# Optimization experiments

Hardware: AMD Instinct MI355X
Metric: run time of the kernel (lower is better)

Reference implementation:

```python
import jax, jax.numpy as jnp
import numpy as np

N_NODES = 100000
N_EDGES = 1600000
F_IN, F_HID, F_OUT = 64, 64, 32


def setup_inputs() -> dict:
    key = jax.random.key(0)
    k1, k2, k3, k4 = jax.random.split(key, 4)
    x = jax.random.normal(k1, (N_NODES, F_IN), dtype=jnp.float32)
    edge_idx = jax.random.randint(k2, (2, N_EDGES), 0, N_NODES, dtype=jnp.int64)
    W1 = jax.random.normal(k3, (F_IN, F_HID), dtype=jnp.float32) * (1.0 / np.sqrt(F_IN))
    b1 = jnp.zeros((F_HID,), dtype=jnp.float32)
    W2 = jax.random.normal(k4, (F_HID, F_OUT), dtype=jnp.float32) * (1.0 / np.sqrt(F_HID))
    b2 = jnp.zeros((F_OUT,), dtype=jnp.float32)
    return {"x": x, "edge_idx": edge_idx, "W1": W1, "b1": b1, "W2": W2, "b2": b2}


def _gcn_conv(h, src, dst, norm, W, b, n):
    # PyG GCNConv: transform first, then normalized sum aggregation, then bias.
    h = h @ W                                   # [N, F_out]
    msg = h[src] * norm[:, None]                # [E+N, F_out] gather + scale
    agg = jax.ops.segment_sum(msg, dst, num_segments=n)  # scatter-add
    return agg + b


def reference(x, edge_idx, W1, b1, W2, b2):
    n = x.shape[0]
    loop = jnp.arange(n, dtype=edge_idx.dtype)
    src = jnp.concatenate([edge_idx[0], loop])  # add self-loops
    dst = jnp.concatenate([edge_idx[1], loop])
    # symmetric normalization D^-1/2 (A+I) D^-1/2
    deg = jax.ops.segment_sum(jnp.ones_like(dst, dtype=x.dtype), dst, num_segments=n)
    dinv = jnp.where(deg > 0, jax.lax.rsqrt(deg), 0.0)
    norm = dinv[src] * dinv[dst]                # [E+N]

    h = _gcn_conv(x, src, dst, norm, W1, b1, n)
    h = jax.nn.relu(h)
    # dropout(p=0.5) is identity in eval mode (deterministic reference)
    out = _gcn_conv(h, src, dst, norm, W2, b2, n)
    return out
```

## Files before the change

kernel.cpp:

```cpp
#include <hip/hip_runtime.h>
#include <hip/hip_bf16.h>
#include <hip/hip_fp16.h>


#define N_FEAT_IN 64
#define B2SHIFT 9
#define CHUNK 4096

struct alignas(8) half4 { __half2 lo, hi; };

__global__ __launch_bounds__(1024) void passA_hist(const int* __restrict__ dst,
                                                   int* __restrict__ H, int E) {
    __shared__ int h[256];
    int t = threadIdx.x;
    if (t < 256) h[t] = 0;
    __syncthreads();
    int base = blockIdx.x * CHUNK;
    int end = min(base + CHUNK, E);
    for (int i = base + t; i < end; i += 1024)
        atomicAdd(&h[dst[i] >> B2SHIFT], 1);
    __syncthreads();
    if (t < 256) H[blockIdx.x * 256 + t] = h[t];
}

__global__ __launch_bounds__(512) void col_scan_a(int* __restrict__ H,
                                                  int* __restrict__ ctot, int NR) {
    __shared__ int s[512];
    int b = blockIdx.x;
    int t = threadIdx.x;
    int v = (t < NR) ? H[t * 256 + b] : 0;
    s[t] = v;
    __syncthreads();
    for (int off = 1; off < 512; off <<= 1) {
        int a = (t >= off) ? s[t - off] : 0;
        __syncthreads();
        s[t] += a;
        __syncthreads();
    }
    if (t < NR) H[t * 256 + b] = s[t] - v;
    if (t == 511) ctot[b] = s[511];
}

__global__ __launch_bounds__(256) void col_scan_b(const int* __restrict__ ctot,
                                                  int* __restrict__ cbase,
                                                  int* __restrict__ bbase,
                                                  int* __restrict__ row_ptr,
                                                  int NB, int n, int E) {
    __shared__ int s[256];
    int t = threadIdx.x;
    int v = ctot[t];
    s[t] = v;
    __syncthreads();
    for (int off = 1; off < 256; off <<= 1) {
        int a = (t >= off) ? s[t - off] : 0;
        __syncthreads();
        s[t] += a;
        __syncthreads();
    }
    int e = s[t] - v;
    cbase[t] = e;
    if (t < NB) bbase[t] = e;
    if (t == 0) { bbase[NB] = E; row_ptr[n] = E; }
}

__global__ __launch_bounds__(1024) void passB_place(const int* __restrict__ src,
                                                    const int* __restrict__ dst,
                                                    const int* __restrict__ H,
                                                    const int* __restrict__ cbase,
                                                    unsigned* __restrict__ bedges, int E) {
    __shared__ int cur[256];
    int t = threadIdx.x;
    if (t < 256) cur[t] = H[blockIdx.x * 256 + t] + cbase[t];
    __syncthreads();
    int base = blockIdx.x * CHUNK;
    int end = min(base + CHUNK, E);
    for (int i = base + t; i < end; i += 1024) {
        int d = dst[i];
        int p = atomicAdd(&cur[d >> B2SHIFT], 1);
        bedges[p] = ((unsigned)src[i] << B2SHIFT) | (unsigned)(d & 511);
    }
}

__global__ __launch_bounds__(1024) void bucket_csr(const int* __restrict__ bbase,
                                                   const unsigned* __restrict__ bedges,
                                                   int* __restrict__ row_ptr,
                                                   float* __restrict__ dinv,
                                                   int* __restrict__ csr_src, int n) {
    __shared__ int lh[512];
    __shared__ int cur[512];
    int t = threadIdx.x;
    if (t < 512) lh[t] = 0;
    __syncthreads();
    int b = blockIdx.x;
    int beg = bbase[b], end = bbase[b + 1];
    for (int i = beg + t; i < end; i += 1024)
        atomicAdd(&lh[bedges[i] & 511], 1);
    __syncthreads();
    int c = (t < 512) ? lh[t] : 0;
    for (int off = 1; off < 512; off <<= 1) {
        int a = (t < 512 && t >= off) ? lh[t - off] : 0;
        __syncthreads();
        if (t < 512) lh[t] += a;
        __syncthreads();
    }
    if (t < 512) {
        int d = (b << B2SHIFT) + t;
        int excl = beg + lh[t] - c;
        cur[t] = excl;
        if (d < n) {
            row_ptr[d] = excl;
            dinv[d] = rsqrtf((float)c + 1.0f);
        }
    }
    __syncthreads();
    for (int i = beg + t; i < end; i += 1024) {
        unsigned v = bedges[i];
        int p = atomicAdd(&cur[v & 511], 1);
        csr_src[p] = (int)(v >> B2SHIFT);
    }
}

__global__ __launch_bounds__(256) void gemm64(const float* __restrict__ A,
                                              const float* __restrict__ W,
                                              const float* __restrict__ dinv,
                                              __half* __restrict__ outh, int n) {
    constexpr int K = 64, FO = 64, CPT = 16;
    __shared__ float As[64][K + 4];
    __shared__ float Ws[K][FO];

    const int t = threadIdx.x;
    const int r0 = blockIdx.x * 64;

    if (blockIdx.x == 0 && t < FO)
        outh[(size_t)n * FO + t] = __float2half(0.f);

    for (int i = t; i < K * FO / 4; i += 256) {
        int k = i / (FO / 4);
        int c4 = (i % (FO / 4)) * 4;
        *(float4*)&Ws[k][c4] = *(const float4*)&W[k * FO + c4];
    }
    for (int i = t; i < 1024; i += 256) {
        int row = i / 16;
        int c4 = (i % 16) * 4;
        int g = r0 + row;
        float4 v = make_float4(0.f, 0.f, 0.f, 0.f);
        if (g < n) v = *(const float4*)&A[(size_t)g * K + c4];
        *(float4*)&As[row][c4] = v;
    }
    __syncthreads();

    const int row = t >> 2;
    const int c0 = (t & 3) * CPT;
    float acc[CPT];
#pragma unroll
    for (int j = 0; j < CPT; ++j) acc[j] = 0.f;
#pragma unroll
    for (int k = 0; k < K; ++k) {
        float xv = As[row][k];
#pragma unroll
        for (int j = 0; j < CPT; ++j) acc[j] = fmaf(xv, Ws[k][c0 + j], acc[j]);
    }

    int g = r0 + row;
    if (g < n) {
        float sc = dinv[g];
#pragma unroll
        for (int j4 = 0; j4 < CPT; j4 += 4) {
            half4 h;
            h.lo = __floats2half2_rn(acc[j4] * sc, acc[j4 + 1] * sc);
            h.hi = __floats2half2_rn(acc[j4 + 2] * sc, acc[j4 + 3] * sc);
            *(half4*)&outh[(size_t)g * FO + c0 + j4] = h;
        }
    }
}

__global__ __launch_bounds__(256) void agg64(const int* __restrict__ row_ptr,
                                             const int* __restrict__ csr_src,
                                             const float* __restrict__ dinv,
                                             const __half* __restrict__ xs1,
                                             const float* __restrict__ b1,
                                             __half* __restrict__ th, int n) {
    int d = blockIdx.x * 16 + (threadIdx.x >> 4);
    if (d >= n) return;
    int c = threadIdx.x & 15;

    int beg = row_ptr[d];
    int end = row_ptr[d + 1];

    half4 sv = *(const half4*)&xs1[(size_t)d * 64 + 4 * c];
    float2 slo = __half22float2(sv.lo), shi = __half22float2(sv.hi);
    float a0 = slo.x, a1 = slo.y, a2 = shi.x, a3 = shi.y;

    for (int jb = beg; jb < end; jb += 8) {
        int idx[8];
#pragma unroll
        for (int k = 0; k < 8; ++k) {
            int j = jb + k;
            int s = csr_src[min(j, end - 1)];
            idx[k] = (j < end) ? s : n;
        }
        half4 v[8];
#pragma unroll
        for (int k = 0; k < 8; ++k)
            v[k] = *(const half4*)&xs1[(size_t)idx[k] * 64 + 4 * c];
#pragma unroll
        for (int k = 0; k < 8; ++k) {
            float2 lo = __half22float2(v[k].lo), hi = __half22float2(v[k].hi);
            a0 += lo.x; a1 += lo.y; a2 += hi.x; a3 += hi.y;
        }
    }

    float di = dinv[d];
    float4 bv = *(const float4*)&b1[4 * c];
    float t0 = fmaxf(fmaf(di, a0, bv.x), 0.f);
    float t1 = fmaxf(fmaf(di, a1, bv.y), 0.f);
    float t2 = fmaxf(fmaf(di, a2, bv.z), 0.f);
    float t3 = fmaxf(fmaf(di, a3, bv.w), 0.f);
    half4 h;
    h.lo = __floats2half2_rn(t0, t1);
    h.hi = __floats2half2_rn(t2, t3);
    *(half4*)&th[(size_t)d * 64 + 4 * c] = h;
}

__global__ __launch_bounds__(256) void gemm32h(const __half* __restrict__ Ah,
                                               const float* __restrict__ W,
                                               const float* __restrict__ dinv,
                                               __half* __restrict__ outh, int n) {
    constexpr int K = 64, FO = 32, CPT = 8;
    __shared__ float As[64][K + 4];
    __shared__ float Ws[K][FO];

    const int t = threadIdx.x;
    const int r0 = blockIdx.x * 64;

    if (blockIdx.x == 0 && t < FO)
        outh[(size_t)n * FO + t] = __float2half(0.f);

    for (int i = t; i < K * FO / 4; i += 256) {
        int k = i / (FO / 4);
        int c4 = (i % (FO / 4)) * 4;
        *(float4*)&Ws[k][c4] = *(const float4*)&W[k * FO + c4];
    }
    for (int i = t; i < 1024; i += 256) {
        int row = i / 16;
        int c4 = (i % 16) * 4;
        int g = r0 + row;
        float4 v = make_float4(0.f, 0.f, 0.f, 0.f);
        if (g < n) {
            half4 hv = *(const half4*)&Ah[(size_t)g * K + c4];
            float2 lo = __half22float2(hv.lo), hi = __half22float2(hv.hi);
            v = make_float4(lo.x, lo.y, hi.x, hi.y);
        }
        *(float4*)&As[row][c4] = v;
    }
    __syncthreads();

    const int row = t >> 2;
    const int c0 = (t & 3) * CPT;
    float acc[CPT];
#pragma unroll
    for (int j = 0; j < CPT; ++j) acc[j] = 0.f;
#pragma unroll
    for (int k = 0; k < K; ++k) {
        float xv = As[row][k];
#pragma unroll
        for (int j = 0; j < CPT; ++j) acc[j] = fmaf(xv, Ws[k][c0 + j], acc[j]);
    }

    int g = r0 + row;
    if (g < n) {
        float sc = dinv[g];
#pragma unroll
        for (int j4 = 0; j4 < CPT; j4 += 4) {
            half4 h;
            h.lo = __floats2half2_rn(acc[j4] * sc, acc[j4 + 1] * sc);
            h.hi = __floats2half2_rn(acc[j4 + 2] * sc, acc[j4 + 3] * sc);
            *(half4*)&outh[(size_t)g * FO + c0 + j4] = h;
        }
    }
}

__global__ __launch_bounds__(256) void agg32(const int* __restrict__ row_ptr,
                                             const int* __restrict__ csr_src,
                                             const float* __restrict__ dinv,
                                             const __half* __restrict__ xs2,
                                             const float* __restrict__ b2,
                                             float* __restrict__ out, int n) {
    int d = blockIdx.x * 32 + (threadIdx.x >> 3);
    if (d >= n) return;
    int c = threadIdx.x & 7;

    int beg = row_ptr[d];
    int end = row_ptr[d + 1];

    half4 sv = *(const half4*)&xs2[(size_t)d * 32 + 4 * c];
    float2 slo = __half22float2(sv.lo), shi = __half22float2(sv.hi);
    float a0 = slo.x, a1 = slo.y, a2 = shi.x, a3 = shi.y;

    for (int jb = beg; jb < end; jb += 8) {
        int idx[8];
#pragma unroll
        for (int k = 0; k < 8; ++k) {
            int j = jb + k;
            int s = csr_src[min(j, end - 1)];
            idx[k] = (j < end) ? s : n;
        }
        half4 v[8];
#pragma unroll
        for (int k = 0; k < 8; ++k)
            v[k] = *(const half4*)&xs2[(size_t)idx[k] * 32 + 4 * c];
#pragma unroll
        for (int k = 0; k < 8; ++k) {
            float2 lo = __half22float2(v[k].lo), hi = __half22float2(v[k].hi);
            a0 += lo.x; a1 += lo.y; a2 += hi.x; a3 += hi.y;
        }
    }

    float di = dinv[d];
    float4 bv = *(const float4*)&b2[4 * c];
    float4 r;
    r.x = fmaf(di, a0, bv.x);
    r.y = fmaf(di, a1, bv.y);
    r.z = fmaf(di, a2, bv.z);
    r.w = fmaf(di, a3, bv.w);
    *(float4*)&out[(size_t)d * 32 + 4 * c] = r;
}

extern "C" void kernel_launch(void* const* d_in, const int* in_sizes, int n_in,
                              void* d_out, int out_size, void* d_ws, size_t ws_size,
                              hipStream_t stream) {
    const float* x  = (const float*)d_in[0];
    const int*   ei = (const int*)d_in[1];
    const float* W1 = (const float*)d_in[2];
    const float* b1 = (const float*)d_in[3];
    const float* W2 = (const float*)d_in[4];
    const float* b2 = (const float*)d_in[5];
    float* out = (float*)d_out;

    const int n = in_sizes[0] / N_FEAT_IN;
    const int E = in_sizes[1] / 2;
    const int* srcI = ei;
    const int* dstI = ei + E;

    const int NB = (n + 511) >> B2SHIFT;
    const int NR = (E + CHUNK - 1) / CHUNK;

    char* ws = (char*)d_ws;
    size_t off = 0;
    auto alloc = [&](size_t bytes) {
        void* p = ws + off;
        off += (bytes + 255) & ~(size_t)255;
        return p;
    };
    float*    dinv    = (float*)alloc((size_t)n * 4);
    int*      row_ptr = (int*)alloc((size_t)(n + 1) * 4);
    int*      bbase   = (int*)alloc((size_t)(NB + 1) * 4);
    int*      ctot    = (int*)alloc((size_t)256 * 4);
    int*      cbase   = (int*)alloc((size_t)256 * 4);
    int*      H       = (int*)alloc((size_t)NR * 256 * 4);
    unsigned* bedges  = (unsigned*)alloc((size_t)E * 4);
    int*      csr_src = (int*)alloc((size_t)E * 4);
    __half*   xs1     = (__half*)alloc((size_t)(n + 1) * 64 * 2);
    __half*   th      = (__half*)alloc((size_t)n * 64 * 2);
    __half*   xs2     = (__half*)alloc((size_t)(n + 1) * 32 * 2);

    passA_hist<<<NR, 1024, 0, stream>>>(dstI, H, E);
    col_scan_a<<<256, 512, 0, stream>>>(H, ctot, NR);
    col_scan_b<<<1, 256, 0, stream>>>(ctot, cbase, bbase, row_ptr, NB, n, E);
    passB_place<<<NR, 1024, 0, stream>>>(srcI, dstI, H, cbase, bedges, E);

    bucket_csr<<<NB, 1024, 0, stream>>>(bbase, bedges, row_ptr, dinv, csr_src, n);

    gemm64<<<(n + 63) / 64, 256, 0, stream>>>(x, W1, dinv, xs1, n);

    agg64<<<(n + 15) / 16, 256, 0, stream>>>(row_ptr, csr_src, dinv, xs1, b1, th, n);

    gemm32h<<<(n + 63) / 64, 256, 0, stream>>>(th, W2, dinv, xs2, n);

    agg32<<<(n + 31) / 32, 256, 0, stream>>>(row_ptr, csr_src, dinv, xs2, b2, out, n);
}
```

Measured before the change: 203.4 us.

## Pad CSR rows to multiples of eight and widen aggregation gathers to 16 bytes

Each destination's neighbor list is padded to a multiple of 8 entries, with the padding pointing at a zero row, and a separate row-end array is kept. The aggregation kernels can then read indices as aligned int4 vectors without bounds checks and prefetch the next index block while gathering. Each thread now handles 8 features using 16-byte half8 loads instead of 4 with 8-byte loads, so fewer threads cover each node. The cost is a larger CSR buffer, extra padding writes in bucket_csr, and more wasted gathers on the padded zero rows.

```diff
diff --git a/kernel.cpp b/kernel.cpp
--- a/kernel.cpp
+++ b/kernel.cpp
@@ -6,8 +6,10 @@
 #define N_FEAT_IN 64
 #define B2SHIFT 9
 #define CHUNK 4096
+#define PADSTRIDE 3592
 
 struct alignas(8) half4 { __half2 lo, hi; };
+struct alignas(16) half8 { __half2 h[4]; };
 
 __global__ __launch_bounds__(1024) void passA_hist(const int* __restrict__ dst,
                                                    int* __restrict__ H, int E) {
@@ -84,6 +86,7 @@
 __global__ __launch_bounds__(1024) void bucket_csr(const int* __restrict__ bbase,
                                                    const unsigned* __restrict__ bedges,
                                                    int* __restrict__ row_ptr,
+                                                   int* __restrict__ rend,
                                                    float* __restrict__ dinv,
                                                    int* __restrict__ csr_src, int n) {
     __shared__ int lh[512];
@@ -97,19 +100,26 @@
         atomicAdd(&lh[bedges[i] & 511], 1);
     __syncthreads();
     int c = (t < 512) ? lh[t] : 0;
+    __syncthreads();
+    int cp = (c + 7) & ~7;
+    if (t < 512) lh[t] = cp;
+    __syncthreads();
     for (int off = 1; off < 512; off <<= 1) {
         int a = (t < 512 && t >= off) ? lh[t - off] : 0;
         __syncthreads();
         if (t < 512) lh[t] += a;
         __syncthreads();
     }
+    int pb = ((beg + 7) & ~7) + b * PADSTRIDE;
     if (t < 512) {
         int d = (b << B2SHIFT) + t;
-        int excl = beg + lh[t] - c;
-        cur[t] = excl;
+        int rbeg = pb + lh[t] - cp;
+        cur[t] = rbeg;
         if (d < n) {
-            row_ptr[d] = excl;
+            row_ptr[d] = rbeg;
+            rend[d] = rbeg + cp;
             dinv[d] = rsqrtf((float)c + 1.0f);
+            for (int i = c; i < cp; ++i) csr_src[rbeg + i] = n;
         }
     }
     __syncthreads();
@@ -174,52 +184,81 @@
     }
 }
 
+#define ACC8(v)                                                       \
+    {                                                                 \
+        float2 f0 = __half22float2((v).h[0]);                         \
+        float2 f1 = __half22float2((v).h[1]);                         \
+        float2 f2 = __half22float2((v).h[2]);                         \
+        float2 f3 = __half22float2((v).h[3]);                         \
+        a0 += f0.x; a1 += f0.y; a2 += f1.x; a3 += f1.y;               \
+        a4 += f2.x; a5 += f2.y; a6 += f3.x; a7 += f3.y;               \
+    }
+
 __global__ __launch_bounds__(256) void agg64(const int* __restrict__ row_ptr,
+                                             const int* __restrict__ rend,
                                              const int* __restrict__ csr_src,
                                              const float* __restrict__ dinv,
                                              const __half* __restrict__ xs1,
                                              const float* __restrict__ b1,
                                              __half* __restrict__ th, int n) {
-    int d = blockIdx.x * 16 + (threadIdx.x >> 4);
+    int d = blockIdx.x * 32 + (threadIdx.x >> 3);
     if (d >= n) return;
-    int c = threadIdx.x & 15;
+    int c = threadIdx.x & 7;
+    const half8* __restrict__ xrow = (const half8*)xs1 + c;
+
+    half8 sv = xrow[(size_t)d * 8];
+    float a0, a1, a2, a3, a4, a5, a6, a7;
+    {
+        float2 f0 = __half22float2(sv.h[0]), f1 = __half22float2(sv.h[1]);
+        float2 f2 = __half22float2(sv.h[2]), f3 = __half22float2(sv.h[3]);
+        a0 = f0.x; a1 = f0.y; a2 = f1.x; a3 = f1.y;
+        a4 = f2.x; a5 = f2.y; a6 = f3.x; a7 = f3.y;
+    }
 
     int beg = row_ptr[d];
-    int end = row_ptr[d + 1];
-
-    half4 sv = *(const half4*)&xs1[(size_t)d * 64 + 4 * c];
-    float2 slo = __half22float2(sv.lo), shi = __half22float2(sv.hi);
-    float a0 = slo.x, a1 = slo.y, a2 = shi.x, a3 = shi.y;
-
-    for (int jb = beg; jb < end; jb += 8) {
-        int idx[8];
-#pragma unroll
-        for (int k = 0; k < 8; ++k) {
-            int j = jb + k;
-            int s = csr_src[min(j, end - 1)];
-            idx[k] = (j < end) ? s : n;
-        }
-        half4 v[8];
-#pragma unroll
-        for (int k = 0; k < 8; ++k)
-            v[k] = *(const half4*)&xs1[(size_t)idx[k] * 64 + 4 * c];
-#pragma unroll
-        for (int k = 0; k < 8; ++k) {
-            float2 lo = __half22float2(v[k].lo), hi = __half22float2(v[k].hi);
-            a0 += lo.x; a1 += lo.y; a2 += hi.x; a3 += hi.y;
+    int end = rend[d];
+    if (beg < end) {
+        int4 ia = *(const int4*)&csr_src[beg];
+        int4 ib = *(const int4*)&csr_src[beg + 4];
+        int jb = beg;
+        for (;;) {
+            int jn = jb + 8;
+            bool more = jn < end;
+            int js = more ? jn : beg;
+            int4 na = *(const int4*)&csr_src[js];
+            int4 nb = *(const int4*)&csr_src[js + 4];
+            half8 v0 = xrow[(size_t)ia.x * 8];
+            half8 v1 = xrow[(size_t)ia.y * 8];
+            half8 v2 = xrow[(size_t)ia.z * 8];
+            half8 v3 = xrow[(size_t)ia.w * 8];
+            half8 v4 = xrow[(size_t)ib.x * 8];
+            half8 v5 = xrow[(size_t)ib.y * 8];
+            half8 v6 = xrow[(size_t)ib.z * 8];
+            half8 v7 = xrow[(size_t)ib.w * 8];
+            ACC8(v0); ACC8(v1); ACC8(v2); ACC8(v3);
+            ACC8(v4); ACC8(v5); ACC8(v6); ACC8(v7);
+            if (!more) break;
+            jb = jn; ia = na; ib = nb;
         }
     }
 
     float di = dinv[d];
-    float4 bv = *(const float4*)&b1[4 * c];
-    float t0 = fmaxf(fmaf(di, a0, bv.x), 0.f);
-    float t1 = fmaxf(fmaf(di, a1, bv.y), 0.f);
-    float t2 = fmaxf(fmaf(di, a2, bv.z), 0.f);
-    float t3 = fmaxf(fmaf(di, a3, bv.w), 0.f);
-    half4 h;
-    h.lo = __floats2half2_rn(t0, t1);
-    h.hi = __floats2half2_rn(t2, t3);
-    *(half4*)&th[(size_t)d * 64 + 4 * c] = h;
+    float4 ba = *(const float4*)&b1[8 * c];
+    float4 bb = *(const float4*)&b1[8 * c + 4];
+    float t0 = fmaxf(fmaf(di, a0, ba.x), 0.f);
+    float t1 = fmaxf(fmaf(di, a1, ba.y), 0.f);
+    float t2 = fmaxf(fmaf(di, a2, ba.z), 0.f);
+    float t3 = fmaxf(fmaf(di, a3, ba.w), 0.f);
+    float t4 = fmaxf(fmaf(di, a4, bb.x), 0.f);
+    float t5 = fmaxf(fmaf(di, a5, bb.y), 0.f);
+    float t6 = fmaxf(fmaf(di, a6, bb.z), 0.f);
+    float t7 = fmaxf(fmaf(di, a7, bb.w), 0.f);
+    half8 o;
+    o.h[0] = __floats2half2_rn(t0, t1);
+    o.h[1] = __floats2half2_rn(t2, t3);
+    o.h[2] = __floats2half2_rn(t4, t5);
+    o.h[3] = __floats2half2_rn(t6, t7);
+    *(half8*)&th[(size_t)d * 64 + 8 * c] = o;
 }
 
 __global__ __launch_bounds__(256) void gemm32h(const __half* __restrict__ Ah,
@@ -281,49 +320,67 @@
 }
 
 __global__ __launch_bounds__(256) void agg32(const int* __restrict__ row_ptr,
+                                             const int* __restrict__ rend,
                                              const int* __restrict__ csr_src,
                                              const float* __restrict__ dinv,
                                              const __half* __restrict__ xs2,
                                              const float* __restrict__ b2,
                                              float* __restrict__ out, int n) {
-    int d = blockIdx.x * 32 + (threadIdx.x >> 3);
+    int d = blockIdx.x * 64 + (threadIdx.x >> 2);
     if (d >= n) return;
-    int c = threadIdx.x & 7;
+    int c = threadIdx.x & 3;
+    const half8* __restrict__ xrow = (const half8*)xs2 + c;
+
+    half8 sv = xrow[(size_t)d * 4];
+    float a0, a1, a2, a3, a4, a5, a6, a7;
+    {
+        float2 f0 = __half22float2(sv.h[0]), f1 = __half22float2(sv.h[1]);
+        float2 f2 = __half22float2(sv.h[2]), f3 = __half22float2(sv.h[3]);
+        a0 = f0.x; a1 = f0.y; a2 = f1.x; a3 = f1.y;
+        a4 = f2.x; a5 = f2.y; a6 = f3.x; a7 = f3.y;
+    }
 
     int beg = row_ptr[d];
-    int end = row_ptr[d + 1];
-
-    half4 sv = *(const half4*)&xs2[(size_t)d * 32 + 4 * c];
-    float2 slo = __half22float2(sv.lo), shi = __half22float2(sv.hi);
-    float a0 = slo.x, a1 = slo.y, a2 = shi.x, a3 = shi.y;
-
-    for (int jb = beg; jb < end; jb += 8) {
-        int idx[8];
-#pragma unroll
-        for (int k = 0; k < 8; ++k) {
-            int j = jb + k;
-            int s = csr_src[min(j, end - 1)];
-            idx[k] = (j < end) ? s : n;
-        }
-        half4 v[8];
-#pragma unroll
-        for (int k = 0; k < 8; ++k)
-            v[k] = *(const half4*)&xs2[(size_t)idx[k] * 32 + 4 * c];
-#pragma unroll
-        for (int k = 0; k < 8; ++k) {
-            float2 lo = __half22float2(v[k].lo), hi = __half22float2(v[k].hi);
-            a0 += lo.x; a1 += lo.y; a2 += hi.x; a3 += hi.y;
+    int end = rend[d];
+    if (beg < end) {
+        int4 ia = *(const int4*)&csr_src[beg];
+        int4 ib = *(const int4*)&csr_src[beg + 4];
+        int jb = beg;
+        for (;;) {
+            int jn = jb + 8;
+            bool more = jn < end;
+            int js = more ? jn : beg;
+            int4 na = *(const int4*)&csr_src[js];
+            int4 nb = *(const int4*)&csr_src[js + 4];
+            half8 v0 = xrow[(size_t)ia.x * 4];
+            half8 v1 = xrow[(size_t)ia.y * 4];
+            half8 v2 = xrow[(size_t)ia.z * 4];
+            half8 v3 = xrow[(size_t)ia.w * 4];
+            half8 v4 = xrow[(size_t)ib.x * 4];
+            half8 v5 = xrow[(size_t)ib.y * 4];
+            half8 v6 = xrow[(size_t)ib.z * 4];
+            half8 v7 = xrow[(size_t)ib.w * 4];
+            ACC8(v0); ACC8(v1); ACC8(v2); ACC8(v3);
+            ACC8(v4); ACC8(v5); ACC8(v6); ACC8(v7);
+            if (!more) break;
+            jb = jn; ia = na; ib = nb;
         }
     }
 
     float di = dinv[d];
-    float4 bv = *(const float4*)&b2[4 * c];
-    float4 r;
-    r.x = fmaf(di, a0, bv.x);
-    r.y = fmaf(di, a1, bv.y);
-    r.z = fmaf(di, a2, bv.z);
-    r.w = fmaf(di, a3, bv.w);
-    *(float4*)&out[(size_t)d * 32 + 4 * c] = r;
+    float4 ba = *(const float4*)&b2[8 * c];
+    float4 bb = *(const float4*)&b2[8 * c + 4];
+    float4 r0, r1;
+    r0.x = fmaf(di, a0, ba.x);
+    r0.y = fmaf(di, a1, ba.y);
+    r0.z = fmaf(di, a2, ba.z);
+    r0.w = fmaf(di, a3, ba.w);
+    r1.x = fmaf(di, a4, bb.x);
+    r1.y = fmaf(di, a5, bb.y);
+    r1.z = fmaf(di, a6, bb.z);
+    r1.w = fmaf(di, a7, bb.w);
+    *(float4*)&out[(size_t)d * 32 + 8 * c] = r0;
+    *(float4*)&out[(size_t)d * 32 + 8 * c + 4] = r1;
 }
 
 extern "C" void kernel_launch(void* const* d_in, const int* in_sizes, int n_in,
@@ -354,12 +411,13 @@
     };
     float*    dinv    = (float*)alloc((size_t)n * 4);
     int*      row_ptr = (int*)alloc((size_t)(n + 1) * 4);
+    int*      rend    = (int*)alloc((size_t)n * 4);
     int*      bbase   = (int*)alloc((size_t)(NB + 1) * 4);
     int*      ctot    = (int*)alloc((size_t)256 * 4);
     int*      cbase   = (int*)alloc((size_t)256 * 4);
     int*      H       = (int*)alloc((size_t)NR * 256 * 4);
     unsigned* bedges  = (unsigned*)alloc((size_t)E * 4);
-    int*      csr_src = (int*)alloc((size_t)E * 4);
+    int*      csr_src = (int*)alloc((size_t)(E + (size_t)NB * PADSTRIDE + 16) * 4);
     __half*   xs1     = (__half*)alloc((size_t)(n + 1) * 64 * 2);
     __half*   th      = (__half*)alloc((size_t)n * 64 * 2);
     __half*   xs2     = (__half*)alloc((size_t)(n + 1) * 32 * 2);
@@ -369,13 +427,13 @@
     col_scan_b<<<1, 256, 0, stream>>>(ctot, cbase, bbase, row_ptr, NB, n, E);
     passB_place<<<NR, 1024, 0, stream>>>(srcI, dstI, H, cbase, bedges, E);
 
-    bucket_csr<<<NB, 1024, 0, stream>>>(bbase, bedges, row_ptr, dinv, csr_src, n);
+    bucket_csr<<<NB, 1024, 0, stream>>>(bbase, bedges, row_ptr, rend, dinv, csr_src, n);
 
     gemm64<<<(n + 63) / 64, 256, 0, stream>>>(x, W1, dinv, xs1, n);
 
-    agg64<<<(n + 15) / 16, 256, 0, stream>>>(row_ptr, csr_src, dinv, xs1, b1, th, n);
+    agg64<<<(n + 31) / 32, 256, 0, stream>>>(row_ptr, rend, csr_src, dinv, xs1, b1, th, n);
 
     gemm32h<<<(n + 63) / 64, 256, 0, stream>>>(th, W2, dinv, xs2, n);
 
-    agg32<<<(n + 31) / 32, 256, 0, stream>>>(row_ptr, csr_src, dinv, xs2, b2, out, n);
-}
+    agg32<<<(n + 63) / 64, 256, 0, stream>>>(row_ptr, rend, csr_src, dinv, xs2, b2, out, n);
+}
```

New measurement: 204.9 us. About the same (+0.8%).
